# Optimization experiments

Measured on AMD Instinct MI355X. Metric: run time of the kernel, lower is better.

## Reference

```python
import jax, jax.numpy as jnp
import numpy as np

LMAX, MMAX = 6, 2
C, COUT = 128, 128
M_SIZE = [LMAX - m + 1 for m in range(MMAX + 1)]  # [7, 6, 5]
LN_EPS = 1e-5


def _perm():
    # l-primary layout (input): for l in 0..lmax, m in -min(l,mmax)..min(l,mmax)
    lp = [(l, m) for l in range(LMAX + 1) for m in range(-min(l, MMAX), min(l, MMAX) + 1)]
    # m-primary layout (CoefficientMapping.to_m): m=0 block, then per m: real(+m) block, imag(-m) block
    mp = [(l, 0) for l in range(LMAX + 1)]
    for m in range(1, MMAX + 1):
        mp += [(l, m) for l in range(m, LMAX + 1)]
        mp += [(l, -m) for l in range(m, LMAX + 1)]
    return np.array([lp.index(t) for t in mp], dtype=np.int32)

PERM = _perm()  # length 29


def setup_inputs() -> dict:
    key = jax.random.key(0)
    ks = jax.random.split(key, 8)
    E = 30000
    num_coeff = sum(2 * min(l, MMAX) + 1 for l in range(LMAX + 1))  # 29
    rad_out = C * sum(M_SIZE)  # 2304 = num_channels_rad
    s = 0.02
    return {
        "x_emb": jax.random.normal(ks[0], (E, num_coeff, C), jnp.float32),
        "x_edge": jax.random.normal(ks[1], (E, C), jnp.float32),
        # RadialFunction: Linear(C,C)+LN+SiLU, Linear(C, rad_out)
        "rad_w1": jax.random.normal(ks[2], (C, C), jnp.float32) * s,
        "rad_b1": jnp.zeros((C,), jnp.float32),
        "rad_g": jnp.ones((C,), jnp.float32),
        "rad_beta": jnp.zeros((C,), jnp.float32),
        "rad_w2": jax.random.normal(ks[3], (rad_out, C), jnp.float32) * s,
        "rad_b2": jnp.ones((rad_out,), jnp.float32),  # gate ~1 so signal survives
        # fc_m0: Linear(7*C, COUT*7, bias=True)
        "w_m0": jax.random.normal(ks[4], (M_SIZE[0] * COUT, M_SIZE[0] * C), jnp.float32) * s,
        "b_m0": jnp.zeros((M_SIZE[0] * COUT,), jnp.float32),
        # SO2_m_Convolution fc for m=1,2: Linear(msz*C, 2*COUT*msz, bias=False)
        "w_m1": jax.random.normal(ks[5], (2 * COUT * M_SIZE[1], M_SIZE[1] * C), jnp.float32) * s,
        "w_m2": jax.random.normal(ks[6], (2 * COUT * M_SIZE[2], M_SIZE[2] * C), jnp.float32) * s,
    }


def reference(x_emb, x_edge, rad_w1, rad_b1, rad_g, rad_beta, rad_w2, rad_b2,
              w_m0, b_m0, w_m1, w_m2):
    E = x_emb.shape[0]
    # _m_primary: permute coefficients from l-primary to m-primary layout
    xm = x_emb[:, PERM, :]  # (E, 29, C)

    # RadialFunction: Linear + LayerNorm + SiLU + Linear
    h = x_edge @ rad_w1.T + rad_b1
    mu = jnp.mean(h, axis=-1, keepdims=True)
    var = jnp.var(h, axis=-1, keepdims=True)
    h = (h - mu) * jax.lax.rsqrt(var + LN_EPS) * rad_g + rad_beta
    h = jax.nn.silu(h)
    rad = h @ rad_w2.T + rad_b2  # (E, 2304)

    # m = 0
    m0 = M_SIZE[0]
    x0 = xm[:, :m0, :].reshape(E, m0 * C)
    x0 = x0 * rad[:, : m0 * C]
    x0 = x0 @ w_m0.T + b_m0  # (E, m0*COUT)
    outs = [x0.reshape(E, m0, COUT)]

    offset, offr = m0, m0 * C
    for msz, w in zip(M_SIZE[1:], (w_m1, w_m2)):
        # (E, 2, msz*C): row 0 = real(+m) coeffs, row 1 = imag(-m) coeffs
        x_m = xm[:, offset:offset + 2 * msz, :].reshape(E, 2, msz * C)
        x_m = x_m * rad[:, offr:offr + msz * C][:, None, :]
        y = jnp.einsum('eki,oi->eko', x_m, w)  # (E, 2, 2*COUT*msz)
        half = w.shape[0] // 2
        y_r, y_i = y[..., :half], y[..., half:]
        out_r = y_r[:, 0:1] - y_i[:, 1:2]
        out_i = y_r[:, 1:2] + y_i[:, 0:1]
        outs.append(jnp.concatenate([out_r, out_i], axis=1).reshape(E, 2 * msz, COUT))
        offset += 2 * msz
        offr += msz * C

    return jnp.concatenate(outs, axis=1)  # (E, 29, COUT), m-primary layout
```

## Files before the change

kernel.cpp:

```cpp
#include <hip/hip_runtime.h>
#include <stdint.h>

typedef unsigned short u16;
typedef __attribute__((ext_vector_type(8))) short short8;
typedef __attribute__((ext_vector_type(8))) u16 u16x8;
typedef __attribute__((ext_vector_type(4))) u16 u16x4;
typedef __attribute__((ext_vector_type(4))) float f32x4;

#define E_TOT 30000
#define TL    3712
#define BM    256
#define BK    64

__constant__ int d_PERM[29] = {0,2,6,11,16,21,26, 3,7,12,17,22,27, 1,5,10,15,20,25,
                               8,13,18,23,28, 4,9,14,19,24};
__constant__ int d_RINV[18][2] = {
  {0,-1},{1,-1},{2,-1},{3,-1},{4,-1},{5,-1},{6,-1},
  {7,13},{8,14},{9,15},{10,16},{11,17},{12,18},
  {19,24},{20,25},{21,26},{22,27},{23,28}};

__device__ __forceinline__ u16 f2bf(float f){
  union { float f; uint32_t u; } v; v.f = f;
  return (u16)((v.u + 0x7FFFu + ((v.u >> 16) & 1u)) >> 16);
}
__device__ __forceinline__ float bf2f(u16 u){
  union { uint32_t u; float f; } v; v.u = ((uint32_t)u) << 16;
  return v.f;
}
__device__ __forceinline__ void gl_lds16(const void* g, void* l){
  __builtin_amdgcn_global_load_lds((const __attribute__((address_space(1))) void*)g,
                                   (__attribute__((address_space(3))) void*)l, 16, 0, 0);
}

__global__ void k_build_w(const float* __restrict__ w0, const float* __restrict__ w1,
                          const float* __restrict__ w2, const float* __restrict__ rw2,
                          u16* __restrict__ W0, u16* __restrict__ W1, u16* __restrict__ W2,
                          u16* __restrict__ w2b){
  int idx = blockIdx.x * 256 + threadIdx.x;
  if (idx < 2304*128){ w2b[idx] = f2bf(rw2[idx]); return; }
  idx -= 2304*128;
  if (idx < 1024*896){
    W0[idx] = (idx < 896*896) ? f2bf(w0[idx]) : (u16)0;
    return;
  }
  idx -= 1024*896;
  if (idx < 1536*1536){
    const int half = 768;
    int o = idx / 1536, i2 = idx - o*1536;
    float v;
    if (o < half) v = (i2 < half) ? w1[o*half + i2] : -w1[(half+o)*half + (i2-half)];
    else { int op = o - half;
           v = (i2 < half) ? w1[(half+op)*half + i2] : w1[op*half + (i2-half)]; }
    W1[idx] = f2bf(v);
    return;
  }
  idx -= 1536*1536;
  if (idx < 1280*1280){
    const int half = 640;
    int o = idx / 1280, i2 = idx - o*1280;
    float v;
    if (o < half) v = (i2 < half) ? w2[o*half + i2] : -w2[(half+o)*half + (i2-half)];
    else { int op = o - half;
           v = (i2 < half) ? w2[(half+op)*half + i2] : w2[op*half + (i2-half)]; }
    W2[idx] = f2bf(v);
  }
}

__global__ __launch_bounds__(256) void k_h(const float* __restrict__ xe,
    const float* __restrict__ w1, const float* __restrict__ b1,
    const float* __restrict__ g, const float* __restrict__ beta,
    u16* __restrict__ hout){
  __shared__ float sw[128*132];
  __shared__ float sxe[16*128];
  int tid = threadIdx.x;
  #pragma unroll
  for (int q = 0; q < 16; q++){
    int i4 = q*256 + tid;
    int row = i4 >> 5, c4 = (i4 & 31) * 4;
    *(f32x4*)&sw[row*132 + c4] = *(const f32x4*)&w1[row*128 + c4];
  }
  int el = tid >> 4, s = tid & 15;
  for (int g8 = 0; g8 < 8; g8++){
    long eb = (long)blockIdx.x * 128 + g8*16;
    if (eb >= E_TOT) break;
    __syncthreads();
    #pragma unroll
    for (int q = 0; q < 2; q++){
      int off = q*1024 + tid*4;
      long er = eb + (off >> 7); if (er > (long)(E_TOT-1)) er = (long)(E_TOT-1);
      *(f32x4*)&sxe[off] = *(const f32x4*)&xe[er*128 + (off & 127)];
    }
    __syncthreads();
    float acc[8];
    #pragma unroll
    for (int q = 0; q < 8; q++) acc[q] = 0.f;
    const float* xr = &sxe[el*128];
    for (int c4 = 0; c4 < 32; c4++){
      f32x4 x = *(const f32x4*)&xr[c4*4];
      #pragma unroll
      for (int q = 0; q < 8; q++){
        f32x4 w = *(const f32x4*)&sw[(s + 16*q)*132 + c4*4];
        acc[q] += x[0]*w[0] + x[1]*w[1] + x[2]*w[2] + x[3]*w[3];
      }
    }
    float sum = 0.f, ss = 0.f;
    #pragma unroll
    for (int q = 0; q < 8; q++){
      acc[q] += b1[s + 16*q];
      sum += acc[q]; ss += acc[q]*acc[q];
    }
    #pragma unroll
    for (int m = 1; m < 16; m <<= 1){ sum += __shfl_xor(sum, m); ss += __shfl_xor(ss, m); }
    float mu = sum * (1.f/128.f);
    float var = ss * (1.f/128.f) - mu*mu;
    float rs = rsqrtf(var + 1e-5f);
    long e = eb + el;
    if (e < (long)E_TOT){
      #pragma unroll
      for (int q = 0; q < 8; q++){
        int j = s + 16*q;
        float v = (acc[q] - mu) * rs * g[j] + beta[j];
        v = v / (1.f + expf(-v));
        hout[e*128 + j] = f2bf(v);
      }
    }
  }
}

__global__ __launch_bounds__(256) void k_radt(
    const u16* __restrict__ h, const u16* __restrict__ w2b,
    const float* __restrict__ b2, const float* __restrict__ xemb,
    u16* __restrict__ t)
{
  __shared__ u16 sH[64*136];
  __shared__ u16 sT[64*72];
  int tid = threadIdx.x;
  long eb = (long)blockIdx.x * 64;
  int nn0 = blockIdx.y * 9;
  #pragma unroll
  for (int q = 0; q < 4; q++){
    int ch = q*256 + tid;
    int row = ch >> 4, col = (ch & 15) * 8;
    long er = eb + row; if (er > (long)(E_TOT-1)) er = (long)(E_TOT-1);
    *(u16x8*)&sH[row*136 + col] = *(const u16x8*)&h[er*128 + col];
  }
  __syncthreads();
  int lane = tid & 63, wid = tid >> 6;
  int wr = wid >> 1, wc = wid & 1;
  int lr = lane & 15, lh = lane >> 4;
  short8 afr[2][4];
  #pragma unroll
  for (int mi = 0; mi < 2; mi++)
    #pragma unroll
    for (int ks = 0; ks < 4; ks++)
      afr[mi][ks] = *(const short8*)&sH[(wr*32 + mi*16 + lr)*136 + ks*32 + lh*8];

  for (int nn = nn0; nn < nn0 + 9; ++nn){
    int nb = nn * 64;
    f32x4 acc[2][2];
    #pragma unroll
    for (int mi = 0; mi < 2; mi++)
      #pragma unroll
      for (int nj = 0; nj < 2; nj++){ acc[mi][nj][0]=0;acc[mi][nj][1]=0;acc[mi][nj][2]=0;acc[mi][nj][3]=0; }
    #pragma unroll
    for (int ks = 0; ks < 4; ks++){
      #pragma unroll
      for (int nj = 0; nj < 2; nj++){
        short8 bf = *(const short8*)&w2b[(long)(nb + wc*32 + nj*16 + lr)*128 + ks*32 + lh*8];
        #pragma unroll
        for (int mi = 0; mi < 2; mi++)
          acc[mi][nj] = __builtin_amdgcn_mfma_f32_16x16x32_bf16(afr[mi][ks], bf, acc[mi][nj], 0, 0, 0);
      }
    }
    __syncthreads();
    #pragma unroll
    for (int mi = 0; mi < 2; mi++){
      #pragma unroll
      for (int nj = 0; nj < 2; nj++){
        int col = wc*32 + nj*16 + lr;
        float bv = b2[nb + col];
        #pragma unroll
        for (int q = 0; q < 4; q++){
          int row = wr*32 + mi*16 + lh*4 + q;
          sT[row*72 + col] = f2bf(acc[mi][nj][q] + bv);
        }
      }
    }
    __syncthreads();
    int rcb = nb >> 7, chalf = nb & 64;
    #pragma unroll
    for (int rr = 0; rr < 2; rr++){
      int r = d_RINV[rcb][rr];
      if (r < 0) break;
      int xrow = d_PERM[r];
      #pragma unroll
      for (int q = 0; q < 2; q++){
        int ch = q*256 + tid;
        int row = ch >> 3, c8 = (ch & 7) * 8;
        long e = eb + row;
        if (e < (long)E_TOT){
          const float* xp = &xemb[(e*29 + xrow)*128 + chalf + c8];
          f32x4 x0 = *(const f32x4*)xp;
          f32x4 x1 = *(const f32x4*)(xp + 4);
          u16x8 rv = *(const u16x8*)&sT[row*72 + c8];
          u16x8 o;
          o[0]=f2bf(x0[0]*bf2f(rv[0])); o[1]=f2bf(x0[1]*bf2f(rv[1]));
          o[2]=f2bf(x0[2]*bf2f(rv[2])); o[3]=f2bf(x0[3]*bf2f(rv[3]));
          o[4]=f2bf(x1[0]*bf2f(rv[4])); o[5]=f2bf(x1[1]*bf2f(rv[5]));
          o[6]=f2bf(x1[2]*bf2f(rv[6])); o[7]=f2bf(x1[3]*bf2f(rv[7]));
          *(u16x8*)&t[(e*29 + r)*128 + chalf + c8] = o;
        }
      }
    }
  }
}

#define WVM6 asm volatile("s_waitcnt vmcnt(6)" ::: "memory");
#define WVM2 asm volatile("s_waitcnt vmcnt(2)" ::: "memory");
#define WVM0 asm volatile("s_waitcnt vmcnt(0)" ::: "memory");
#define BARR __builtin_amdgcn_s_barrier();
#define SB0  __builtin_amdgcn_sched_barrier(0);

#define READ_A(buf, QM)                                                       \
  _Pragma("unroll")                                                           \
  for (int i = 0; i < 4; i++){                                                \
    _Pragma("unroll")                                                         \
    for (int ks = 0; ks < 2; ks++)                                            \
      af[i][ks] = *(const short8*)&S[buf][0][(wr*128 + (QM)*64 + i*16 + lr)*64\
                                            + ((ks*32 + lh*8) ^ swz)];        \
  }
#define READ_B(dst, buf, QN)                                                  \
  _Pragma("unroll")                                                           \
  for (int j = 0; j < 2; j++){                                                \
    _Pragma("unroll")                                                         \
    for (int ks = 0; ks < 2; ks++)                                            \
      dst[j][ks] = *(const short8*)&S[buf][1][(wc*64 + (QN)*32 + j*16 + lr)*64\
                                              + ((ks*32 + lh*8) ^ swz)];      \
  }
#define MFMA16(QM, QN, bfr)                                                   \
  __builtin_amdgcn_s_setprio(1);                                              \
  _Pragma("unroll")                                                           \
  for (int i = 0; i < 4; i++){                                                \
    _Pragma("unroll")                                                         \
    for (int j = 0; j < 2; j++){                                              \
      _Pragma("unroll")                                                       \
      for (int ks = 0; ks < 2; ks++)                                          \
        acc[(QM)*4+i][(QN)*2+j] = __builtin_amdgcn_mfma_f32_16x16x32_bf16(    \
            af[i][ks], bfr[j][ks], acc[(QM)*4+i][(QN)*2+j], 0, 0, 0);         \
    }                                                                         \
  }                                                                           \
  __builtin_amdgcn_s_setprio(0);

#define STAGE_EARLY(pn)                                                       \
  { _Pragma("unroll")                                                         \
    for (int k2 = 0; k2 < 6; k2++){                                           \
      gl_lds16(gsrc[k2], l0 + ((pn) << 15) + ldso[k2]);                       \
      gsrc[k2] += 64;                                                         \
    } }
#define STAGE_LATE(pn)                                                        \
  { _Pragma("unroll")                                                         \
    for (int k2 = 6; k2 < 8; k2++){                                           \
      gl_lds16(gsrc[k2], l0 + ((pn) << 15) + ldso[k2]);                       \
      gsrc[k2] += 64;                                                         \
    } }

__global__ __launch_bounds__(512, 2) void k_gemm8(
    const u16* __restrict__ A,
    const u16* __restrict__ W0, const u16* __restrict__ W1, const u16* __restrict__ W2,
    const float* __restrict__ bias0,
    float* __restrict__ out)
{
  __shared__ u16 S[2][2][BM*BK];

  int orig = blockIdx.x;
  int xcd = orig & 7, idxs = orig >> 3;
  int wgid = (xcd < 2 ? xcd*222 : 444 + (xcd-2)*221) + idxs;

  int ntn, K, kbase, nvalid, base;
  const u16* Wg; const float* bias = nullptr;
  if (wgid < 472)      { base=0;    ntn=4; K=896;  kbase=0;    nvalid=896;  Wg=W0; bias=bias0; }
  else if (wgid < 1180){ base=472;  ntn=6; K=1536; kbase=896;  nvalid=1536; Wg=W1; }
  else                 { base=1180; ntn=5; K=1280; kbase=2432; nvalid=1280; Wg=W2; }
  int local = wgid - base;
  int ncol = (local % ntn) * 256;
  int mrow = (local / ntn) * 256;
  int nkt  = K >> 6;

  int tid = threadIdx.x;
  int lane = tid & 63, wid = tid >> 6;
  int wr = wid >> 2, wc = wid & 3;
  int lr = lane & 15, lh = lane >> 4;
  int swz = (lane & 7) << 3;

  const u16* gsrc[8];
  int ldso[8];
  u16* l0 = &S[0][0][0];
  #pragma unroll
  for (int j = 0; j < 2; j++){
    int CH = (wid*2 + j)*64 + lane;
    int c16 = CH & 7;
    int ra0 = ((CH >> 9) << 7) + ((CH >> 3) & 63);
    long g0 = mrow + ra0; if (g0 > (long)(E_TOT-1)) g0 = (long)(E_TOT-1);
    gsrc[2+j] = A + g0*(long)TL + kbase + ((c16 ^ (ra0 & 7)) << 3);
    ldso[2+j] = ra0*64 + c16*8;
    int ra1 = ra0 + 64;
    long g1 = mrow + ra1; if (g1 > (long)(E_TOT-1)) g1 = (long)(E_TOT-1);
    gsrc[6+j] = A + g1*(long)TL + kbase + ((c16 ^ (ra1 & 7)) << 3);
    ldso[6+j] = ra1*64 + c16*8;
    int rb0 = ((CH >> 8) << 6) + ((CH >> 3) & 31);
    gsrc[0+j] = Wg + (long)(ncol + rb0)*K + ((c16 ^ (rb0 & 7)) << 3);
    ldso[0+j] = 16384 + rb0*64 + c16*8;
    int rb1 = rb0 + 32;
    gsrc[4+j] = Wg + (long)(ncol + rb1)*K + ((c16 ^ (rb1 & 7)) << 3);
    ldso[4+j] = 16384 + rb1*64 + c16*8;
  }

  f32x4 acc[8][4];
  #pragma unroll
  for (int i = 0; i < 8; i++)
    #pragma unroll
    for (int j = 0; j < 4; j++){ acc[i][j][0]=0;acc[i][j][1]=0;acc[i][j][2]=0;acc[i][j][3]=0; }

  short8 af[4][2];
  short8 b0[2][2];
  short8 b1[2][2];

  STAGE_EARLY(0)
  STAGE_LATE(0)
  WVM2 BARR SB0
  READ_A(0, 0)
  READ_B(b0, 0, 0)
  READ_B(b1, 0, 1)

  for (int t = 0; t < nkt-1; ++t){
    int p = t & 1, pn = p ^ 1;
    STAGE_EARLY(pn)
    MFMA16(0,0,b0)
    MFMA16(0,1,b1)
    WVM6 BARR SB0
    READ_A(p, 1)
    STAGE_LATE(pn)
    MFMA16(1,1,b1)
    MFMA16(1,0,b0)
    WVM2 BARR SB0
    READ_A(pn, 0)
    READ_B(b0, pn, 0)
    READ_B(b1, pn, 1)
  }
  {
    int p = (nkt-1) & 1;
    MFMA16(0,0,b0)
    MFMA16(0,1,b1)
    WVM0 BARR SB0
    READ_A(p, 1)
    MFMA16(1,1,b1)
    MFMA16(1,0,b0)
  }

  #pragma unroll
  for (int mi = 0; mi < 8; mi++){
    #pragma unroll
    for (int nj = 0; nj < 4; nj++){
      int col = wc*64 + nj*16 + lr;
      if (ncol + col < nvalid){
        float bv = bias ? bias[ncol + col] : 0.f;
        #pragma unroll
        for (int q = 0; q < 4; q++){
          long row = mrow + wr*128 + mi*16 + lh*4 + q;
          if (row < E_TOT)
            out[row*(long)TL + kbase + ncol + col] = acc[mi][nj][q] + bv;
        }
      }
    }
  }
}

extern "C" void kernel_launch(void* const* d_in, const int* in_sizes, int n_in,
                              void* d_out, int out_size, void* d_ws, size_t ws_size,
                              hipStream_t stream){
  (void)in_sizes; (void)n_in; (void)out_size;
  const float* x_emb  = (const float*)d_in[0];
  const float* x_edge = (const float*)d_in[1];
  const float* rad_w1 = (const float*)d_in[2];
  const float* rad_b1 = (const float*)d_in[3];
  const float* rad_g  = (const float*)d_in[4];
  const float* rad_bt = (const float*)d_in[5];
  const float* rad_w2 = (const float*)d_in[6];
  const float* rad_b2 = (const float*)d_in[7];
  const float* w_m0   = (const float*)d_in[8];
  const float* b_m0   = (const float*)d_in[9];
  const float* w_m1   = (const float*)d_in[10];
  const float* w_m2   = (const float*)d_in[11];
  float* out = (float*)d_out;
  char* ws = (char*)d_ws;

  u16* t   = (u16*)(ws + 0);
  u16* h   = (u16*)(ws + 222720000);
  u16* W0  = (u16*)(ws + 230400000);
  u16* W1  = (u16*)(ws + 232235008);
  u16* W2  = (u16*)(ws + 236953600);
  u16* w2b = (u16*)(ws + 240230400);
  if (ws_size < 240820224ull) return;

  k_build_w<<<dim3(20352), dim3(256), 0, stream>>>(w_m0, w_m1, w_m2, rad_w2,
                                                   W0, W1, W2, w2b);
  k_h<<<dim3(235), dim3(256), 0, stream>>>(x_edge, rad_w1, rad_b1, rad_g, rad_bt, h);
  k_radt<<<dim3(469, 4), dim3(256), 0, stream>>>(h, w2b, rad_b2, x_emb, t);
  k_gemm8<<<dim3(1770), dim3(512), 0, stream>>>(t, W0, W1, W2, b_m0, out);
}
```

Baseline: 662.6 us.

## Restructure GEMM main loop into fine-grained 8-phase staged pipeline

Replaces the two-phase double-buffered K loop with a schedule that splits each tile's global-to-LDS staging into four slots interleaved with four MFMA quarter-blocks, separated by barriers. The next buffer is prefetched deeper (slot 3 ahead) and the loop is unrolled by two tiles, with semi and bare epilogue tiles. The aim is better overlap of global loads, LDS reads and MFMA work. The cost is many more workgroup barriers, and it assumes nkt is even, which holds for K of 896, 1536 and 1280.

Measured after the change: 836.1 us. 1.26x slower.

```diff
diff --git a/kernel.cpp b/kernel.cpp
--- a/kernel.cpp
+++ b/kernel.cpp
@@ -216,10 +216,9 @@
 }
 
 #define WVM6 asm volatile("s_waitcnt vmcnt(6)" ::: "memory");
-#define WVM2 asm volatile("s_waitcnt vmcnt(2)" ::: "memory");
 #define WVM0 asm volatile("s_waitcnt vmcnt(0)" ::: "memory");
-#define BARR __builtin_amdgcn_s_barrier();
-#define SB0  __builtin_amdgcn_sched_barrier(0);
+#define CF   asm volatile("" ::: "memory");
+#define BAR  CF __builtin_amdgcn_s_barrier(); CF
 
 #define READ_A(buf, QM)                                                       \
   _Pragma("unroll")                                                           \
@@ -251,18 +250,70 @@
   }                                                                           \
   __builtin_amdgcn_s_setprio(0);
 
-#define STAGE_EARLY(pn)                                                       \
+#define STG(slot, bufc)                                                       \
   { _Pragma("unroll")                                                         \
-    for (int k2 = 0; k2 < 6; k2++){                                           \
-      gl_lds16(gsrc[k2], l0 + ((pn) << 15) + ldso[k2]);                       \
-      gsrc[k2] += 64;                                                         \
+    for (int j2 = 0; j2 < 2; j2++){                                           \
+      gl_lds16(gsrc[(slot)*2+j2], l0 + (bufc)*32768 + ldso[(slot)*2+j2]);     \
+      gsrc[(slot)*2+j2] += 64;                                                \
     } }
-#define STAGE_LATE(pn)                                                        \
-  { _Pragma("unroll")                                                         \
-    for (int k2 = 6; k2 < 8; k2++){                                           \
-      gl_lds16(gsrc[k2], l0 + ((pn) << 15) + ldso[k2]);                       \
-      gsrc[k2] += 64;                                                         \
-    } }
+
+#define TILE_FULL(P, PN)                                                      \
+  READ_A(P, 0)                                                                \
+  READ_B(b0, P, 0)                                                            \
+  STG(3, PN)                                                                  \
+  BAR                                                                         \
+  MFMA16(0,0,b0)                                                              \
+  BAR                                                                         \
+  READ_B(b1, P, 1)                                                            \
+  STG(0, P)                                                                   \
+  BAR                                                                         \
+  MFMA16(0,1,b1)                                                              \
+  BAR                                                                         \
+  READ_A(P, 1)                                                                \
+  STG(1, P)                                                                   \
+  BAR                                                                         \
+  MFMA16(1,1,b1)                                                              \
+  BAR                                                                         \
+  STG(2, P)                                                                   \
+  WVM6                                                                        \
+  BAR                                                                         \
+  MFMA16(1,0,b0)                                                              \
+  BAR
+
+#define TILE_SEMI(P, PN)                                                      \
+  READ_A(P, 0)                                                                \
+  READ_B(b0, P, 0)                                                            \
+  STG(3, PN)                                                                  \
+  BAR                                                                         \
+  MFMA16(0,0,b0)                                                              \
+  BAR                                                                         \
+  READ_B(b1, P, 1)                                                            \
+  BAR                                                                         \
+  MFMA16(0,1,b1)                                                              \
+  BAR                                                                         \
+  READ_A(P, 1)                                                                \
+  BAR                                                                         \
+  MFMA16(1,1,b1)                                                              \
+  BAR                                                                         \
+  WVM0                                                                        \
+  BAR                                                                         \
+  MFMA16(1,0,b0)                                                              \
+  BAR
+
+#define TILE_BARE(P)                                                          \
+  READ_A(P, 0)                                                                \
+  READ_B(b0, P, 0)                                                            \
+  BAR                                                                         \
+  MFMA16(0,0,b0)                                                              \
+  BAR                                                                         \
+  READ_B(b1, P, 1)                                                            \
+  BAR                                                                         \
+  MFMA16(0,1,b1)                                                              \
+  BAR                                                                         \
+  READ_A(P, 1)                                                                \
+  BAR                                                                         \
+  MFMA16(1,1,b1)                                                              \
+  MFMA16(1,0,b0)
 
 __global__ __launch_bounds__(512, 2) void k_gemm8(
     const u16* __restrict__ A,
@@ -301,15 +352,15 @@
     int c16 = CH & 7;
     int ra0 = ((CH >> 9) << 7) + ((CH >> 3) & 63);
     long g0 = mrow + ra0; if (g0 > (long)(E_TOT-1)) g0 = (long)(E_TOT-1);
-    gsrc[2+j] = A + g0*(long)TL + kbase + ((c16 ^ (ra0 & 7)) << 3);
-    ldso[2+j] = ra0*64 + c16*8;
+    gsrc[0+j] = A + g0*(long)TL + kbase + ((c16 ^ (ra0 & 7)) << 3);
+    ldso[0+j] = ra0*64 + c16*8;
     int ra1 = ra0 + 64;
     long g1 = mrow + ra1; if (g1 > (long)(E_TOT-1)) g1 = (long)(E_TOT-1);
     gsrc[6+j] = A + g1*(long)TL + kbase + ((c16 ^ (ra1 & 7)) << 3);
     ldso[6+j] = ra1*64 + c16*8;
     int rb0 = ((CH >> 8) << 6) + ((CH >> 3) & 31);
-    gsrc[0+j] = Wg + (long)(ncol + rb0)*K + ((c16 ^ (rb0 & 7)) << 3);
-    ldso[0+j] = 16384 + rb0*64 + c16*8;
+    gsrc[2+j] = Wg + (long)(ncol + rb0)*K + ((c16 ^ (rb0 & 7)) << 3);
+    ldso[2+j] = 16384 + rb0*64 + c16*8;
     int rb1 = rb0 + 32;
     gsrc[4+j] = Wg + (long)(ncol + rb1)*K + ((c16 ^ (rb1 & 7)) << 3);
     ldso[4+j] = 16384 + rb1*64 + c16*8;
@@ -325,37 +376,18 @@
   short8 b0[2][2];
   short8 b1[2][2];
 
-  STAGE_EARLY(0)
-  STAGE_LATE(0)
-  WVM2 BARR SB0
-  READ_A(0, 0)
-  READ_B(b0, 0, 0)
-  READ_B(b1, 0, 1)
-
-  for (int t = 0; t < nkt-1; ++t){
-    int p = t & 1, pn = p ^ 1;
-    STAGE_EARLY(pn)
-    MFMA16(0,0,b0)
-    MFMA16(0,1,b1)
-    WVM6 BARR SB0
-    READ_A(p, 1)
-    STAGE_LATE(pn)
-    MFMA16(1,1,b1)
-    MFMA16(1,0,b0)
-    WVM2 BARR SB0
-    READ_A(pn, 0)
-    READ_B(b0, pn, 0)
-    READ_B(b1, pn, 1)
-  }
-  {
-    int p = (nkt-1) & 1;
-    MFMA16(0,0,b0)
-    MFMA16(0,1,b1)
-    WVM0 BARR SB0
-    READ_A(p, 1)
-    MFMA16(1,1,b1)
-    MFMA16(1,0,b0)
-  }
+  STG(0,0) STG(1,0) STG(2,0) STG(3,0)
+  STG(0,1) STG(1,1) STG(2,1)
+  WVM6
+  BAR
+
+  int npair = (nkt >> 1) - 1;
+  for (int u = 0; u < npair; ++u){
+    TILE_FULL(0, 1)
+    TILE_FULL(1, 0)
+  }
+  TILE_SEMI(0, 1)
+  TILE_BARE(1)
 
   #pragma unroll
   for (int mi = 0; mi < 8; mi++){
```
